# Performance work log

Measured on AMD Instinct MI355X. Metric: run time of the kernel, lower is better.

Reference implementation:

```python
import jax, jax.numpy as jnp
import numpy as np

N_NODES = 100000
N_EDGES = 625000
D_IN = 128
D_HID = 256


def setup_inputs() -> dict:
    key = jax.random.key(0)
    ks = jax.random.split(key, 9)
    x = jax.random.normal(ks[0], (N_NODES, D_IN), dtype=jnp.float32)
    edge_index = jax.random.randint(ks[1], (2, N_EDGES), 0, N_NODES, dtype=jnp.int64)
    s = 1.0 / np.sqrt(D_IN)
    # SAGEConv params: lin_l applied to mean-aggregated neighbors (with bias),
    # lin_r applied to root features (no bias) -- PyG defaults.
    w_l = jax.random.uniform(ks[2], (D_IN, D_HID), minval=-s, maxval=s, dtype=jnp.float32)
    b_l = jax.random.uniform(ks[3], (D_HID,), minval=-s, maxval=s, dtype=jnp.float32)
    w_r = jax.random.uniform(ks[4], (D_IN, D_HID), minval=-s, maxval=s, dtype=jnp.float32)
    sh = 1.0 / np.sqrt(D_HID)
    w_p = jax.random.uniform(ks[5], (D_HID, 7), minval=-sh, maxval=sh, dtype=jnp.float32)
    b_p = jax.random.uniform(ks[6], (7,), minval=-sh, maxval=sh, dtype=jnp.float32)
    w_s = jax.random.uniform(ks[7], (D_HID, 6), minval=-sh, maxval=sh, dtype=jnp.float32)
    b_s = jax.random.uniform(ks[8], (6,), minval=-sh, maxval=sh, dtype=jnp.float32)
    return {"x": x, "edge_index": edge_index, "w_l": w_l, "b_l": b_l, "w_r": w_r,
            "w_p": w_p, "b_p": b_p, "w_s": w_s, "b_s": b_s}


def reference(x, edge_index, w_l, b_l, w_r, w_p, b_p, w_s, b_s):
    src, dst = edge_index[0], edge_index[1]
    n = x.shape[0]
    # SAGEConv mean aggregation: mean of source-node features over each target
    agg = jax.ops.segment_sum(x[src], dst, num_segments=n)          # [N, D_IN]
    cnt = jax.ops.segment_sum(jnp.ones(src.shape, x.dtype), dst, num_segments=n)
    mean = agg / jnp.maximum(cnt, 1.0)[:, None]                      # isolated nodes -> 0
    h = mean @ w_l + b_l + x @ w_r                                   # [N, D_HID]
    h = jax.nn.relu(h)                                               # dropout = identity (eval)
    pr = h @ w_p + b_p                                               # [N, 7]
    sv = h @ w_s + b_s                                               # [N, 6]
    return jax.nn.log_softmax(pr, axis=1), jax.nn.log_softmax(sv, axis=1)
```

## Files before the change

### kernel.cpp

```cpp
#include <hip/hip_runtime.h>
#include <hip/hip_bf16.h>
#include <math.h>

#define NN 100000
#define NE 625000
#define DIN 128
#define DH 256
#define NROWS 100096
#define CAP 32

#define HS_STRIDE 264

#define EDGE_BLOCKS  2442
#define XCAST_BLOCKS 12500
#define PACKW_BLOCKS 32
#define PACKH_BLOCKS 2
#define PREP_BLOCKS  (EDGE_BLOCKS + XCAST_BLOCKS + PACKW_BLOCKS + PACKH_BLOCKS)

typedef __attribute__((ext_vector_type(8))) short bf16x8;
typedef __attribute__((ext_vector_type(4))) float f32x4;
typedef __attribute__((ext_vector_type(4))) unsigned int u32x4;

__device__ __forceinline__ unsigned short f2bf(float f) {
    unsigned u = __builtin_bit_cast(unsigned, f);
    u += 0x7fffu + ((u >> 16) & 1u);
    return (unsigned short)(u >> 16);
}
__device__ __forceinline__ unsigned short f2bfu(unsigned u) {
    u += 0x7fffu + ((u >> 16) & 1u);
    return (unsigned short)(u >> 16);
}
__device__ __forceinline__ float bflo(unsigned u) {
    return __builtin_bit_cast(float, u << 16);
}
__device__ __forceinline__ float bfhi(unsigned u) {
    return __builtin_bit_cast(float, u & 0xffff0000u);
}

__device__ __forceinline__ void gll16(const unsigned short* g, unsigned short* l) {
    __builtin_amdgcn_global_load_lds(
        (const __attribute__((address_space(1))) unsigned int*)(const void*)g,
        (__attribute__((address_space(3))) unsigned int*)(void*)l, 16, 0, 0);
}

__global__ __launch_bounds__(256)
void prep(const float* __restrict__ x, const int* __restrict__ ei,
          const float* __restrict__ w_l, const float* __restrict__ w_r,
          const float* __restrict__ w_p, const float* __restrict__ w_s,
          const float* __restrict__ b_p, const float* __restrict__ b_s,
          unsigned short* __restrict__ X, unsigned short* __restrict__ Bp,
          unsigned short* __restrict__ whp, float* __restrict__ bhc,
          int* __restrict__ deg, int* __restrict__ elist) {
    const int b = blockIdx.x;
    const int t = threadIdx.x;

    if (b < EDGE_BLOCKS) {
        int e = b * 256 + t;
        if (e < NE) {
            int dst = __builtin_nontemporal_load(ei + NE + e);
            int src = __builtin_nontemporal_load(ei + e);
            int pos = atomicAdd(&deg[dst], 1);
            if (pos < CAP) elist[dst * CAP + pos] = src;
        }
    } else if (b < EDGE_BLOCKS + XCAST_BLOCKS) {
        int idx = (b - EDGE_BLOCKS) * 256 + t;
        int n = idx >> 5;
        int j4 = (idx & 31) * 4;
        u32x4 v = __builtin_nontemporal_load(
            reinterpret_cast<const u32x4*>(x + (size_t)n * DIN + j4));
        ushort4 o = { f2bfu(v.x), f2bfu(v.y), f2bfu(v.z), f2bfu(v.w) };
        *reinterpret_cast<ushort4*>(X + (size_t)n * 128 + j4) = o;
    } else if (b < EDGE_BLOCKS + XCAST_BLOCKS + PACKW_BLOCKS) {
        int tid = (b - EDGE_BLOCKS - XCAST_BLOCKS) * 256 + t;
        int kt = tid >> 10;
        int ct = (tid >> 6) & 15;
        int L = tid & 63;
        int k0 = kt * 32 + (L >> 4) * 8;
        int c = ct * 16 + (L & 15);
        unsigned short v[8];
#pragma unroll
        for (int j = 0; j < 8; ++j) {
            int k = k0 + j;
            float w = (k < 128) ? w_l[k * 256 + c] : w_r[(k - 128) * 256 + c];
            v[j] = f2bf(w);
        }
        int g = ((ct >> 3) << 6) + (kt << 3) + (ct & 7);
        *reinterpret_cast<bf16x8*>(Bp + (size_t)(g * 64 + L) * 8) =
            *reinterpret_cast<const bf16x8*>(v);
    } else {
        int tid = (b - EDGE_BLOCKS - XCAST_BLOCKS - PACKW_BLOCKS) * 256 + t;
        int kt = tid >> 6;
        int L = tid & 63;
        int k0 = kt * 32 + (L >> 4) * 8;
        int c = L & 15;
        unsigned short v[8];
#pragma unroll
        for (int j = 0; j < 8; ++j) {
            int k = k0 + j;
            float w = (c < 7) ? w_p[k * 7 + c] : (c < 13 ? w_s[k * 6 + (c - 7)] : 0.f);
            v[j] = f2bf(w);
        }
        *reinterpret_cast<bf16x8*>(whp + (size_t)tid * 8) =
            *reinterpret_cast<const bf16x8*>(v);
        if (tid < 16)
            bhc[tid] = (tid < 7) ? b_p[tid] : (tid < 13 ? b_s[tid - 7] : 0.f);
        if (tid >= 16 && tid < 32) {
            uint4 z = {0u, 0u, 0u, 0u};
            *reinterpret_cast<uint4*>(X + (size_t)NN * 128 + (tid - 16) * 8) = z;
        }
    }
}

__device__ __forceinline__ void gacc8(float* m, const uint4& v) {
    m[0] += bflo(v.x); m[1] += bfhi(v.x);
    m[2] += bflo(v.y); m[3] += bfhi(v.y);
    m[4] += bflo(v.z); m[5] += bfhi(v.z);
    m[6] += bflo(v.w); m[7] += bfhi(v.w);
}

__global__ __launch_bounds__(256, 8)
void gather_mean(const unsigned short* __restrict__ X,
                 unsigned short* __restrict__ M,
                 const int* __restrict__ elist,
                 const int* __restrict__ deg) {
    const int t = threadIdx.x;
    const int h = t & 7;
    const int n = blockIdx.x * 32 + (t >> 3);

    const int d = deg[n];
    const int dl = (d < CAP) ? d : CAP;
    const int dpad = (dl + 1) & ~1;
    const int base = n * CAP;

    float macc[16];
#pragma unroll
    for (int j = 0; j < 16; ++j) macc[j] = 0.f;

    int s0 = elist[base + 0];
    int s1 = elist[base + 1];
    s0 = (dl > 0) ? s0 : NN;
    s1 = (dl > 1) ? s1 : NN;

    for (int i = 0; i < dpad; i += 2) {
        const unsigned short* xr0 = X + (size_t)s0 * 128 + h * 16;
        const unsigned short* xr1 = X + (size_t)s1 * 128 + h * 16;
        uint4 a0 = *reinterpret_cast<const uint4*>(xr0);
        uint4 a1 = *reinterpret_cast<const uint4*>(xr0 + 8);
        uint4 b0 = *reinterpret_cast<const uint4*>(xr1);
        uint4 b1 = *reinterpret_cast<const uint4*>(xr1 + 8);
        const int i2 = i + 2;
        int t0 = elist[base + (i2 & 31)];
        int t1 = elist[base + ((i2 + 1) & 31)];
        t0 = (i2 < dl) ? t0 : NN;
        t1 = (i2 + 1 < dl) ? t1 : NN;
        gacc8(macc, a0);
        gacc8(macc + 8, a1);
        gacc8(macc, b0);
        gacc8(macc + 8, b1);
        s0 = t0; s1 = t1;
    }

    const float invd = (dl > 0) ? 1.f / (float)dl : 0.f;
    u32x4 w0, w1;
#pragma unroll
    for (int j = 0; j < 4; ++j) {
        unsigned lo = f2bf(macc[2 * j] * invd);
        unsigned hi = f2bf(macc[2 * j + 1] * invd);
        w0[j] = lo | (hi << 16);
        unsigned lo2 = f2bf(macc[8 + 2 * j] * invd);
        unsigned hi2 = f2bf(macc[8 + 2 * j + 1] * invd);
        w1[j] = lo2 | (hi2 << 16);
    }
    unsigned short* mrow = M + (size_t)n * 128 + h * 16;
    __builtin_nontemporal_store(w0, reinterpret_cast<u32x4*>(mrow));
    __builtin_nontemporal_store(w1, reinterpret_cast<u32x4*>(mrow + 8));
}

__global__ __launch_bounds__(512, 4)
void sage_gemm_fused(const unsigned short* __restrict__ X,
                     const unsigned short* __restrict__ M,
                     const unsigned short* __restrict__ Bp,
                     const float* __restrict__ b_l,
                     const unsigned short* __restrict__ whp,
                     const float* __restrict__ bhc,
                     float* __restrict__ out) {
    __shared__ __align__(16) unsigned char smem[76288];
    unsigned short* Bs = (unsigned short*)smem;
    unsigned short* hs = (unsigned short*)smem;
    float* o13 = (float*)(smem + 67584);

    const int t = threadIdx.x;
    const int wave = t >> 6;
    const int L = t & 63;
    const int q = L >> 4;
    const int m15 = L & 15;
    const int node0 = blockIdx.x * 128;
    const int node = node0 + wave * 16 + m15;

#pragma unroll
    for (int rr = 0; rr < 8; ++rr)
        gll16(Bp + (size_t)(rr * 512 + t) * 8,
              Bs + (size_t)(rr * 512 + (wave << 6)) * 8);

    const unsigned short* mrow = M + (size_t)node * 128;
    const unsigned short* xrow = X + (size_t)node * 128;
    bf16x8 afrag[8];
#pragma unroll
    for (int kt = 0; kt < 4; ++kt)
        afrag[kt] = *reinterpret_cast<const bf16x8*>(mrow + kt * 32 + q * 8);
#pragma unroll
    for (int kt = 4; kt < 8; ++kt)
        afrag[kt] = *reinterpret_cast<const bf16x8*>(xrow + (kt - 4) * 32 + q * 8);

    f32x4 acc[16];
#pragma unroll
    for (int ct = 0; ct < 16; ++ct) acc[ct] = (f32x4){0.f, 0.f, 0.f, 0.f};

    __syncthreads();

#pragma unroll
    for (int kt = 0; kt < 8; ++kt) {
#pragma unroll
        for (int c7 = 0; c7 < 8; ++c7) {
            bf16x8 b = *reinterpret_cast<const bf16x8*>(
                Bs + ((size_t)(kt * 8 + c7) * 64 + L) * 8);
            acc[c7] = __builtin_amdgcn_mfma_f32_16x16x32_bf16(afrag[kt], b, acc[c7], 0, 0, 0);
        }
    }

    __syncthreads();

#pragma unroll
    for (int rr = 0; rr < 8; ++rr)
        gll16(Bp + 32768 + (size_t)(rr * 512 + t) * 8,
              Bs + (size_t)(rr * 512 + (wave << 6)) * 8);
    __syncthreads();

#pragma unroll
    for (int kt = 0; kt < 8; ++kt) {
#pragma unroll
        for (int c7 = 0; c7 < 8; ++c7) {
            bf16x8 b = *reinterpret_cast<const bf16x8*>(
                Bs + ((size_t)(kt * 8 + c7) * 64 + L) * 8);
            acc[8 + c7] = __builtin_amdgcn_mfma_f32_16x16x32_bf16(afrag[kt], b, acc[8 + c7], 0, 0, 0);
        }
    }

    __syncthreads();

#pragma unroll
    for (int ct = 0; ct < 16; ++ct) {
        const int c = ct * 16 + m15;
        const float blv = b_l[c];
        const int r0 = wave * 16 + q * 4;
#pragma unroll
        for (int rr = 0; rr < 4; ++rr)
            hs[(r0 + rr) * HS_STRIDE + c] = f2bf(fmaxf(acc[ct][rr] + blv, 0.f));
    }
    __syncthreads();

    {
        f32x4 acch = (f32x4){0.f, 0.f, 0.f, 0.f};
        const unsigned short* hrow = hs + (size_t)(wave * 16 + m15) * HS_STRIDE;
#pragma unroll
        for (int kt = 0; kt < 8; ++kt) {
            bf16x8 ah = *reinterpret_cast<const bf16x8*>(hrow + kt * 32 + q * 8);
            bf16x8 bh = *reinterpret_cast<const bf16x8*>(whp + ((size_t)(kt * 64 + L)) * 8);
            acch = __builtin_amdgcn_mfma_f32_16x16x32_bf16(ah, bh, acch, 0, 0, 0);
        }
        if (m15 < 13) {
            const float bh = bhc[m15];
#pragma unroll
            for (int rr = 0; rr < 4; ++rr)
                o13[(wave * 16 + q * 4 + rr) * 17 + m15] = acch[rr] + bh;
        }
    }
    __syncthreads();

    if (t < 128) {
        const int gnode = node0 + t;
        if (gnode < NN) {
            float v[7], mx = -1e30f;
#pragma unroll
            for (int j = 0; j < 7; ++j) { v[j] = o13[t * 17 + j]; mx = fmaxf(mx, v[j]); }
            float sum = 0.f;
#pragma unroll
            for (int j = 0; j < 7; ++j) sum += expf(v[j] - mx);
            const float lse = mx + logf(sum);
#pragma unroll
            for (int j = 0; j < 7; ++j) out[(size_t)gnode * 7 + j] = v[j] - lse;

            float u[6], mx2 = -1e30f;
#pragma unroll
            for (int j = 0; j < 6; ++j) { u[j] = o13[t * 17 + 7 + j]; mx2 = fmaxf(mx2, u[j]); }
            float sum2 = 0.f;
#pragma unroll
            for (int j = 0; j < 6; ++j) sum2 += expf(u[j] - mx2);
            const float lse2 = mx2 + logf(sum2);
#pragma unroll
            for (int j = 0; j < 6; ++j) out[(size_t)NN * 7 + (size_t)gnode * 6 + j] = u[j] - lse2;
        }
    }
}

extern "C" void kernel_launch(void* const* d_in, const int* in_sizes, int n_in,
                              void* d_out, int out_size, void* d_ws, size_t ws_size,
                              hipStream_t stream) {
    const float* x   = (const float*)d_in[0];
    const int*   ei  = (const int*)d_in[1];
    const float* w_l = (const float*)d_in[2];
    const float* b_l = (const float*)d_in[3];
    const float* w_r = (const float*)d_in[4];
    const float* w_p = (const float*)d_in[5];
    const float* b_p = (const float*)d_in[6];
    const float* w_s = (const float*)d_in[7];
    const float* b_s = (const float*)d_in[8];
    float* out = (float*)d_out;

    unsigned short* X   = (unsigned short*)d_ws;
    unsigned short* M   = X + (size_t)NROWS * 128;
    unsigned short* Bp  = M + (size_t)NROWS * 128;
    unsigned short* whp = Bp + 65536;
    float* bhc  = (float*)(whp + 4096);
    int* deg    = (int*)(bhc + 16);
    int* elist  = deg + NN;

    hipMemsetAsync(deg, 0, NN * sizeof(int), stream);

    prep<<<PREP_BLOCKS, 256, 0, stream>>>(x, ei, w_l, w_r, w_p, w_s, b_p, b_s,
                                          X, Bp, whp, bhc, deg, elist);

    gather_mean<<<NN / 32, 256, 0, stream>>>(X, M, elist, deg);

    sage_gemm_fused<<<NROWS / 128, 512, 0, stream>>>(X, M, Bp, b_l, whp, bhc, out);
}
```

Before: 203.3 us.

## Fuse neighbor mean gather into the GEMM kernel via shared memory

The separate gather_mean kernel is removed. Each GEMM block now computes the mean aggregation for its 128 nodes, stages the bf16 result in LDS with a padded stride, and builds the A fragments from there, so the M buffer is never written to or read back from global memory and one launch disappears. The prep kernel also switches from nontemporal loads to plain loads for edges and x, and uses a nontemporal store for elist. Trade-off: the irregular gather now runs inside a 512-thread GEMM block with limited occupancy, which may hide latency less well than the dedicated kernel did.

```diff
diff --git a/kernel.cpp b/kernel.cpp
--- a/kernel.cpp
+++ b/kernel.cpp
@@ -10,6 +10,7 @@
 #define CAP 32
 
 #define HS_STRIDE 264
+#define MEAN_STRIDE 136
 
 #define EDGE_BLOCKS  2442
 #define XCAST_BLOCKS 12500
@@ -23,10 +24,6 @@
 
 __device__ __forceinline__ unsigned short f2bf(float f) {
     unsigned u = __builtin_bit_cast(unsigned, f);
-    u += 0x7fffu + ((u >> 16) & 1u);
-    return (unsigned short)(u >> 16);
-}
-__device__ __forceinline__ unsigned short f2bfu(unsigned u) {
     u += 0x7fffu + ((u >> 16) & 1u);
     return (unsigned short)(u >> 16);
 }
@@ -57,18 +54,18 @@
     if (b < EDGE_BLOCKS) {
         int e = b * 256 + t;
         if (e < NE) {
-            int dst = __builtin_nontemporal_load(ei + NE + e);
-            int src = __builtin_nontemporal_load(ei + e);
+            int dst = ei[NE + e];
+            int src = ei[e];
             int pos = atomicAdd(&deg[dst], 1);
-            if (pos < CAP) elist[dst * CAP + pos] = src;
+            if (pos < CAP)
+                __builtin_nontemporal_store(src, elist + dst * CAP + pos);
         }
     } else if (b < EDGE_BLOCKS + XCAST_BLOCKS) {
         int idx = (b - EDGE_BLOCKS) * 256 + t;
         int n = idx >> 5;
         int j4 = (idx & 31) * 4;
-        u32x4 v = __builtin_nontemporal_load(
-            reinterpret_cast<const u32x4*>(x + (size_t)n * DIN + j4));
-        ushort4 o = { f2bfu(v.x), f2bfu(v.y), f2bfu(v.z), f2bfu(v.w) };
+        float4 v = *reinterpret_cast<const float4*>(x + (size_t)n * DIN + j4);
+        ushort4 o = { f2bf(v.x), f2bf(v.y), f2bf(v.z), f2bf(v.w) };
         *reinterpret_cast<ushort4*>(X + (size_t)n * 128 + j4) = o;
     } else if (b < EDGE_BLOCKS + XCAST_BLOCKS + PACKW_BLOCKS) {
         int tid = (b - EDGE_BLOCKS - XCAST_BLOCKS) * 256 + t;
@@ -118,74 +115,18 @@
     m[6] += bflo(v.w); m[7] += bfhi(v.w);
 }
 
-__global__ __launch_bounds__(256, 8)
-void gather_mean(const unsigned short* __restrict__ X,
-                 unsigned short* __restrict__ M,
-                 const int* __restrict__ elist,
-                 const int* __restrict__ deg) {
-    const int t = threadIdx.x;
-    const int h = t & 7;
-    const int n = blockIdx.x * 32 + (t >> 3);
-
-    const int d = deg[n];
-    const int dl = (d < CAP) ? d : CAP;
-    const int dpad = (dl + 1) & ~1;
-    const int base = n * CAP;
-
-    float macc[16];
-#pragma unroll
-    for (int j = 0; j < 16; ++j) macc[j] = 0.f;
-
-    int s0 = elist[base + 0];
-    int s1 = elist[base + 1];
-    s0 = (dl > 0) ? s0 : NN;
-    s1 = (dl > 1) ? s1 : NN;
-
-    for (int i = 0; i < dpad; i += 2) {
-        const unsigned short* xr0 = X + (size_t)s0 * 128 + h * 16;
-        const unsigned short* xr1 = X + (size_t)s1 * 128 + h * 16;
-        uint4 a0 = *reinterpret_cast<const uint4*>(xr0);
-        uint4 a1 = *reinterpret_cast<const uint4*>(xr0 + 8);
-        uint4 b0 = *reinterpret_cast<const uint4*>(xr1);
-        uint4 b1 = *reinterpret_cast<const uint4*>(xr1 + 8);
-        const int i2 = i + 2;
-        int t0 = elist[base + (i2 & 31)];
-        int t1 = elist[base + ((i2 + 1) & 31)];
-        t0 = (i2 < dl) ? t0 : NN;
-        t1 = (i2 + 1 < dl) ? t1 : NN;
-        gacc8(macc, a0);
-        gacc8(macc + 8, a1);
-        gacc8(macc, b0);
-        gacc8(macc + 8, b1);
-        s0 = t0; s1 = t1;
-    }
-
-    const float invd = (dl > 0) ? 1.f / (float)dl : 0.f;
-    u32x4 w0, w1;
-#pragma unroll
-    for (int j = 0; j < 4; ++j) {
-        unsigned lo = f2bf(macc[2 * j] * invd);
-        unsigned hi = f2bf(macc[2 * j + 1] * invd);
-        w0[j] = lo | (hi << 16);
-        unsigned lo2 = f2bf(macc[8 + 2 * j] * invd);
-        unsigned hi2 = f2bf(macc[8 + 2 * j + 1] * invd);
-        w1[j] = lo2 | (hi2 << 16);
-    }
-    unsigned short* mrow = M + (size_t)n * 128 + h * 16;
-    __builtin_nontemporal_store(w0, reinterpret_cast<u32x4*>(mrow));
-    __builtin_nontemporal_store(w1, reinterpret_cast<u32x4*>(mrow + 8));
-}
-
 __global__ __launch_bounds__(512, 4)
-void sage_gemm_fused(const unsigned short* __restrict__ X,
-                     const unsigned short* __restrict__ M,
-                     const unsigned short* __restrict__ Bp,
-                     const float* __restrict__ b_l,
-                     const unsigned short* __restrict__ whp,
-                     const float* __restrict__ bhc,
-                     float* __restrict__ out) {
+void sage_fused(const unsigned short* __restrict__ X,
+                const unsigned short* __restrict__ Bp,
+                const float* __restrict__ b_l,
+                const unsigned short* __restrict__ whp,
+                const float* __restrict__ bhc,
+                const int* __restrict__ elist,
+                const int* __restrict__ deg,
+                float* __restrict__ out) {
     __shared__ __align__(16) unsigned char smem[76288];
     unsigned short* Bs = (unsigned short*)smem;
+    unsigned short* mean_lds = (unsigned short*)smem;
     unsigned short* hs = (unsigned short*)smem;
     float* o13 = (float*)(smem + 67584);
 
@@ -197,24 +138,83 @@
     const int node0 = blockIdx.x * 128;
     const int node = node0 + wave * 16 + m15;
 
+    for (int p = 0; p < 2; ++p) {
+        const int rl = p * 64 + (t >> 3);
+        const int n = node0 + rl;
+        const int h = t & 7;
+        const int d = (n < NN) ? deg[n] : 0;
+        const int dl = (d < CAP) ? d : CAP;
+        const int dpad = (dl + 1) & ~1;
+        const int base = (n < NN ? n : 0) * CAP;
+
+        float macc[16];
+#pragma unroll
+        for (int j = 0; j < 16; ++j) macc[j] = 0.f;
+
+        int s0 = elist[base + 0];
+        int s1 = elist[base + 1];
+        s0 = (dl > 0) ? s0 : NN;
+        s1 = (dl > 1) ? s1 : NN;
+
+        for (int i = 0; i < dpad; i += 2) {
+            const unsigned short* xr0 = X + (size_t)s0 * 128 + h * 16;
+            const unsigned short* xr1 = X + (size_t)s1 * 128 + h * 16;
+            uint4 a0 = *reinterpret_cast<const uint4*>(xr0);
+            uint4 a1 = *reinterpret_cast<const uint4*>(xr0 + 8);
+            uint4 b0 = *reinterpret_cast<const uint4*>(xr1);
+            uint4 b1 = *reinterpret_cast<const uint4*>(xr1 + 8);
+            const int i2 = i + 2;
+            int t0 = elist[base + (i2 & 31)];
+            int t1 = elist[base + ((i2 + 1) & 31)];
+            t0 = (i2 < dl) ? t0 : NN;
+            t1 = (i2 + 1 < dl) ? t1 : NN;
+            gacc8(macc, a0);
+            gacc8(macc + 8, a1);
+            gacc8(macc, b0);
+            gacc8(macc + 8, b1);
+            s0 = t0; s1 = t1;
+        }
+
+        const float invd = (dl > 0) ? 1.f / (float)dl : 0.f;
+        u32x4 w0, w1;
+#pragma unroll
+        for (int j = 0; j < 4; ++j) {
+            unsigned lo = f2bf(macc[2 * j] * invd);
+            unsigned hi = f2bf(macc[2 * j + 1] * invd);
+            w0[j] = lo | (hi << 16);
+            unsigned lo2 = f2bf(macc[8 + 2 * j] * invd);
+            unsigned hi2 = f2bf(macc[8 + 2 * j + 1] * invd);
+            w1[j] = lo2 | (hi2 << 16);
+        }
+        unsigned short* mrow = mean_lds + rl * MEAN_STRIDE + h * 16;
+        *reinterpret_cast<u32x4*>(mrow) = w0;
+        *reinterpret_cast<u32x4*>(mrow + 8) = w1;
+    }
+
+    __syncthreads();
+
+    bf16x8 afrag[8];
+    {
+        const unsigned short* mrow = mean_lds + (size_t)(wave * 16 + m15) * MEAN_STRIDE;
+#pragma unroll
+        for (int kt = 0; kt < 4; ++kt)
+            afrag[kt] = *reinterpret_cast<const bf16x8*>(mrow + kt * 32 + q * 8);
+        const unsigned short* xrow = X + (size_t)node * 128;
+#pragma unroll
+        for (int kt = 4; kt < 8; ++kt)
+            afrag[kt] = *reinterpret_cast<const bf16x8*>(xrow + (kt - 4) * 32 + q * 8);
+    }
+
+    f32x4 acc[16];
+#pragma unroll
+    for (int ct = 0; ct < 16; ++ct) acc[ct] = (f32x4){0.f, 0.f, 0.f, 0.f};
+
+    __syncthreads();
+
 #pragma unroll
     for (int rr = 0; rr < 8; ++rr)
         gll16(Bp + (size_t)(rr * 512 + t) * 8,
               Bs + (size_t)(rr * 512 + (wave << 6)) * 8);
-
-    const unsigned short* mrow = M + (size_t)node * 128;
-    const unsigned short* xrow = X + (size_t)node * 128;
-    bf16x8 afrag[8];
-#pragma unroll
-    for (int kt = 0; kt < 4; ++kt)
-        afrag[kt] = *reinterpret_cast<const bf16x8*>(mrow + kt * 32 + q * 8);
-#pragma unroll
-    for (int kt = 4; kt < 8; ++kt)
-        afrag[kt] = *reinterpret_cast<const bf16x8*>(xrow + (kt - 4) * 32 + q * 8);
-
-    f32x4 acc[16];
-#pragma unroll
-    for (int ct = 0; ct < 16; ++ct) acc[ct] = (f32x4){0.f, 0.f, 0.f, 0.f};
 
     __syncthreads();
 
@@ -318,8 +318,7 @@
     float* out = (float*)d_out;
 
     unsigned short* X   = (unsigned short*)d_ws;
-    unsigned short* M   = X + (size_t)NROWS * 128;
-    unsigned short* Bp  = M + (size_t)NROWS * 128;
+    unsigned short* Bp  = X + (size_t)NROWS * 128;
     unsigned short* whp = Bp + 65536;
     float* bhc  = (float*)(whp + 4096);
     int* deg    = (int*)(bhc + 16);
@@ -330,7 +329,6 @@
     prep<<<PREP_BLOCKS, 256, 0, stream>>>(x, ei, w_l, w_r, w_p, w_s, b_p, b_s,
                                           X, Bp, whp, bhc, deg, elist);
 
-    gather_mean<<<NN / 32, 256, 0, stream>>>(X, M, elist, deg);
-
-    sage_gemm_fused<<<NROWS / 128, 512, 0, stream>>>(X, M, Bp, b_l, whp, bhc, out);
-}
+    sage_fused<<<NROWS / 128, 512, 0, stream>>>(X, Bp, b_l, whp, bhc,
+                                                elist, deg, out);
+}
```

Measured after the change: 197.5 us (median of 2 runs). 1.03x faster.
